# Kernel optimization log

Hardware: AMD Instinct MI355X
Metric: run time of the kernel (lower is better)

## Reference

```python
import jax, jax.numpy as jnp
import numpy as np

THR = 0.5
IOU_THR = 0.2
K = 4096          # fixed pre-NMS candidate budget (jit-compatible stand-in for thr filtering + full sort)
FEAT_OFF = 5      # cols: 0 obj score, 1:5 box (l,t,r,b), 5: class-feature embedding


def setup_inputs() -> dict:
    key = jax.random.key(0)
    kx, kl, kt, kw, kh, ks, kp, kr = jax.random.split(key, 8)
    C, H, W = 261, 320, 320  # 5 + 256 feature channels
    x = jax.random.normal(kx, (1, C, H, W), dtype=jnp.float32)
    # plausible (l,t,r,b) boxes in padded-image coordinates so NMS has real work
    l = jax.random.uniform(kl, (1, 1, H, W), dtype=jnp.float32) * 600.0
    t = jax.random.uniform(kt, (1, 1, H, W), dtype=jnp.float32) * 600.0
    r = l + jax.random.uniform(kw, (1, 1, H, W), dtype=jnp.float32) * 60.0
    b = t + jax.random.uniform(kh, (1, 1, H, W), dtype=jnp.float32) * 60.0
    x = x.at[:, 1:5].set(jnp.concatenate([l, t, r, b], axis=1))
    state_matrix = jax.random.normal(ks, (16, 256), dtype=jnp.float32)
    padding = jax.random.uniform(kp, (2,), dtype=jnp.float32) * 10.0
    ratio = jax.random.uniform(kr, (1,), dtype=jnp.float32) * 0.6 + 0.4
    return {"x": x, "state_matrix": state_matrix, "padding": padding,
            "ratio": ratio, "image_width": 1280, "image_height": 768}


def _pairwise_iou(boxes, eps=1e-10):
    # boxes: [K, 4] as (l, t, r, b); returns [K, K]
    l, t, r, b = boxes[:, 0], boxes[:, 1], boxes[:, 2], boxes[:, 3]
    area = (r - l) * (b - t)
    iw = jnp.clip(jnp.minimum(r[:, None], r[None, :]) - jnp.maximum(l[:, None], l[None, :]), 0.0)
    ih = jnp.clip(jnp.minimum(b[:, None], b[None, :]) - jnp.maximum(t[:, None], t[None, :]), 0.0)
    inter = iw * ih
    union = area[:, None] + area[None, :] - inter + eps
    return inter / union


def reference(x, state_matrix, padding, ratio, image_width, image_height):
    B, C, H, W = x.shape
    out = x[0].reshape(C, H * W).T                      # [N, C]
    sig = jax.nn.sigmoid(out[:, 0])                     # sigmoid on objectness channel
    cls_logits = out[:, FEAT_OFF:] @ state_matrix.T     # [N, 16] class-state matmul
    cls_val = jnp.max(cls_logits, axis=1)
    cls_idx = jnp.argmax(cls_logits, axis=1)
    score = sig * cls_val                               # out[:,0] * cls_values
    valid = sig > THR                                   # out[0] > thr filter
    score = jnp.where(valid, score, -jnp.inf)
    topv, topi = jax.lax.top_k(score, K)                # descending sort, fixed budget
    boxes = out[topi, 1:5]                              # [K, 4] (l,t,r,b)
    cls_k = cls_idx[topi]
    area = (boxes[:, 2] - boxes[:, 0]) * (boxes[:, 3] - boxes[:, 1])
    iou = _pairwise_iou(boxes)                          # [K, K]

    alive0 = jnp.isfinite(topv)                         # only thr-passing candidates enter the queue
    kept0 = jnp.zeros((K,), dtype=bool)

    def body(carry, i):
        alive, kept = carry
        is_cur = alive[i]                               # still in the queue (not suppressed earlier)
        alive = alive.at[i].set(False)                  # pop top
        ious_i = iou[i]
        n_over = jnp.sum((ious_i >= IOU_THR) & alive)   # remaining boxes with iou >= thr
        accept = is_cur & (area[i] >= 4.0) & (n_over >= 10)
        kept = kept.at[i].set(accept)
        alive = jnp.where(accept, alive & (ious_i < IOU_THR), alive)  # suppress only on accept
        return (alive, kept), None

    (_, kept), _ = jax.lax.scan(body, (alive0, kept0), jnp.arange(K))

    keep = kept & (topv >= THR)                         # p[0,0] < thr -> skip
    inv_r = 1.0 / ratio[0]
    x1 = jnp.maximum((boxes[:, 0] - padding[0]) * inv_r, 0.0)
    y1 = jnp.maximum((boxes[:, 1] - padding[1]) * inv_r, 0.0)
    x2 = jnp.minimum((boxes[:, 2] - padding[0]) * inv_r, jnp.float32(image_width))
    y2 = jnp.minimum((boxes[:, 3] - padding[1]) * inv_r, jnp.float32(image_height))
    keep = keep & (x1 < image_width) & (y1 < image_height)

    dets = jnp.stack([jnp.ones((K,), jnp.float32), topv, x1, y1, x2, y2,
                      cls_k.astype(jnp.float32)], axis=1)   # [K, 7]
    dets = jnp.where(keep[:, None], dets, 0.0)
    return dets
```

## Files before the change

### kernel.cpp

```cpp
#include <hip/hip_runtime.h>
#include <hip/hip_bf16.h>
#include <math.h>

#define HW 102400
#define KSEL 4096
#define CAP 16384

__device__ inline unsigned fkey(float f) {
    unsigned u = __float_as_uint(f);
    return (u & 0x80000000u) ? ~u : (u | 0x80000000u);
}

__device__ inline unsigned wave_sum64_s(unsigned x) {
    x += (unsigned)__builtin_amdgcn_update_dpp(0, (int)x, 0x111, 0xf, 0xf, false);
    x += (unsigned)__builtin_amdgcn_update_dpp(0, (int)x, 0x112, 0xf, 0xf, false);
    x += (unsigned)__builtin_amdgcn_update_dpp(0, (int)x, 0x114, 0xf, 0xf, false);
    x += (unsigned)__builtin_amdgcn_update_dpp(0, (int)x, 0x118, 0xf, 0xf, false);
    x += (unsigned)__builtin_amdgcn_update_dpp(0, (int)x, 0x142, 0xa, 0xf, false);
    x += (unsigned)__builtin_amdgcn_update_dpp(0, (int)x, 0x143, 0xc, 0xf, false);
    return (unsigned)__builtin_amdgcn_readlane((int)x, 63);
}

__device__ inline unsigned long long readlane64(unsigned long long v, int l) {
    unsigned lo = (unsigned)__builtin_amdgcn_readlane((int)(unsigned)(v & 0xffffffffull), l);
    unsigned hi = (unsigned)__builtin_amdgcn_readlane((int)(unsigned)(v >> 32), l);
    return ((unsigned long long)hi << 32) | lo;
}

__global__ __launch_bounds__(128) void k_score(const float* __restrict__ x,
                                               const float* __restrict__ sm,
                                               float* __restrict__ score,
                                               int* __restrict__ clsidx,
                                               unsigned* __restrict__ hist) {
    __shared__ float swt[256][16];
    __shared__ float tile[2][16][128];
    int t = threadIdx.x;
    for (int i = t; i < 4096; i += 128) {
        int k = i >> 8, c = i & 255;
        swt[c][k] = sm[i];
    }
    int cg = t >> 5;
    int le = t & 31;
    size_t pxb = (size_t)blockIdx.x * 128;
    const float* xc = x + (size_t)5 * HW + pxb;

    float acc[16];
#pragma unroll
    for (int k = 0; k < 16; ++k) acc[k] = 0.f;

    float4 sa[4], sb[4];

#define LOADX(dst, ti)                                                         \
    _Pragma("unroll") for (int j = 0; j < 4; ++j)                              \
        dst[j] = *(const float4*)(xc + (size_t)((ti) * 16 + 4 * j + cg) * HW + le * 4);
#define STOREX(src, s)                                                         \
    _Pragma("unroll") for (int j = 0; j < 4; ++j)                              \
        ((float4*)&tile[s][4 * j + cg][0])[le] = src[j];
#define COMP(s, ti)                                                            \
    _Pragma("unroll") for (int cc = 0; cc < 16; ++cc) {                        \
        float xv = tile[s][cc][t];                                             \
        const float4* w4 = (const float4*)&swt[(ti) * 16 + cc][0];             \
        float4 w0 = w4[0], w1 = w4[1], w2 = w4[2], w3 = w4[3];                 \
        acc[0]  = fmaf(xv, w0.x, acc[0]);  acc[1]  = fmaf(xv, w0.y, acc[1]);   \
        acc[2]  = fmaf(xv, w0.z, acc[2]);  acc[3]  = fmaf(xv, w0.w, acc[3]);   \
        acc[4]  = fmaf(xv, w1.x, acc[4]);  acc[5]  = fmaf(xv, w1.y, acc[5]);   \
        acc[6]  = fmaf(xv, w1.z, acc[6]);  acc[7]  = fmaf(xv, w1.w, acc[7]);   \
        acc[8]  = fmaf(xv, w2.x, acc[8]);  acc[9]  = fmaf(xv, w2.y, acc[9]);   \
        acc[10] = fmaf(xv, w2.z, acc[10]); acc[11] = fmaf(xv, w2.w, acc[11]);  \
        acc[12] = fmaf(xv, w3.x, acc[12]); acc[13] = fmaf(xv, w3.y, acc[13]);  \
        acc[14] = fmaf(xv, w3.z, acc[14]); acc[15] = fmaf(xv, w3.w, acc[15]);  \
    }

    LOADX(sa, 0);
    STOREX(sa, 0);
    LOADX(sa, 1);
    LOADX(sb, 2);
    __syncthreads();

#pragma unroll
    for (int k = 0; k < 16; k += 2) {
        COMP(k & 1, k);
        STOREX(sa, (k + 1) & 1);
        if (k + 3 < 16) LOADX(sa, k + 3);
        __syncthreads();
        COMP((k + 1) & 1, k + 1);
        if (k + 2 < 16) { STOREX(sb, k & 1); }
        if (k + 4 < 16) LOADX(sb, k + 4);
        __syncthreads();
    }
#undef LOADX
#undef STOREX
#undef COMP

    float mv = acc[0]; int mi = 0;
#pragma unroll
    for (int k = 1; k < 16; ++k)
        if (acc[k] > mv) { mv = acc[k]; mi = k; }
    int n = (int)pxb + t;
    float x0 = x[n];
    float sig = 1.0f / (1.0f + expf(-x0));
    float sc = (sig > 0.5f) ? sig * mv : -INFINITY;
    score[n] = sc;
    clsidx[n] = mi;
    if (sc != -INFINITY) atomicAdd(&hist[fkey(sc) >> 16], 1u);
}

__global__ __launch_bounds__(1024) void k_findp(const unsigned* __restrict__ hist,
                                                unsigned* __restrict__ meta) {
    __shared__ unsigned part[1024];
    __shared__ unsigned sgrp, s_after;
    __shared__ unsigned bins[64];
    int t = threadIdx.x;
    if (t == 0) { sgrp = 0; s_after = 0; }
    unsigned s = 0;
    const unsigned* hp = hist + t * 64;
    for (int i = 0; i < 64; ++i) s += hp[i];
    part[t] = s;
    __syncthreads();
    for (int off = 1; off < 1024; off <<= 1) {
        unsigned v = (t + off < 1024) ? part[t + off] : 0u;
        __syncthreads();
        part[t] += v;
        __syncthreads();
    }
    if (part[t] >= KSEL && (t == 1023 || part[t + 1] < KSEL)) {
        sgrp = (unsigned)t;
        s_after = (t == 1023) ? 0u : part[t + 1];
    }
    __syncthreads();
    unsigned g = sgrp, SA = s_after;
    if (t < 64) bins[t] = hist[g * 64 + t];
    __syncthreads();
    if (t == 0) {
        unsigned acc = SA, p = g * 64;
        for (int b = 63; b >= 0; --b) {
            acc += bins[b];
            if (acc >= KSEL) { p = g * 64 + (unsigned)b; break; }
        }
        meta[1] = p;
    }
}

__global__ void k_collect(const float* __restrict__ score,
                          unsigned* __restrict__ meta,
                          unsigned long long* __restrict__ cand) {
    int n = blockIdx.x * 256 + threadIdx.x;
    unsigned key = fkey(score[n]);
    if ((key >> 16) >= meta[1]) {
        unsigned pos = atomicAdd(&meta[0], 1u);
        if (pos < CAP)
            cand[pos] = ((unsigned long long)key << 32) | (unsigned)(~(unsigned)n);
    }
}

__global__ __launch_bounds__(256) void k_rank(const unsigned long long* __restrict__ cand,
                                              const unsigned* __restrict__ meta,
                                              const float* __restrict__ x,
                                              const float* __restrict__ score,
                                              const int* __restrict__ clsidx,
                                              float* __restrict__ topv,
                                              float* __restrict__ bl, float* __restrict__ bt,
                                              float* __restrict__ br, float* __restrict__ bb,
                                              float* __restrict__ area, int* __restrict__ clsk) {
    __shared__ unsigned long long tile[1024];
    int C = (int)meta[0]; if (C > CAP) C = CAP;
    int j = blockIdx.x * 256 + threadIdx.x;
    unsigned long long kj = (j < C) ? cand[j] : 0ull;
    unsigned rank = 0;
    for (int tb = 0; tb < C; tb += 1024) {
        int cnt = min(1024, C - tb);
        __syncthreads();
        for (int u = threadIdx.x; u < cnt; u += 256) tile[u] = cand[tb + u];
        __syncthreads();
        if (j < C)
            for (int u = 0; u < cnt; ++u) rank += (tile[u] > kj) ? 1u : 0u;
    }
    if (j < C && rank < KSEL) {
        unsigned n = ~(unsigned)(kj & 0xFFFFFFFFull);
        float l  = x[(size_t)1 * HW + n];
        float tt = x[(size_t)2 * HW + n];
        float r  = x[(size_t)3 * HW + n];
        float b  = x[(size_t)4 * HW + n];
        topv[rank] = score[n];
        bl[rank] = l; bt[rank] = tt; br[rank] = r; bb[rank] = b;
        area[rank] = (r - l) * (b - tt);
        clsk[rank] = clsidx[n];
    }
}

__global__ __launch_bounds__(256) void k_mask(const float* __restrict__ bl, const float* __restrict__ bt,
                                              const float* __restrict__ br, const float* __restrict__ bb,
                                              const float* __restrict__ area,
                                              unsigned long long* __restrict__ mask) {
    __shared__ float sl[256], st[256], sr[256], sb[256], sa[256];
    int t = threadIdx.x;
    int ic = blockIdx.x >> 4;
    int jc = blockIdx.x & 15;
    int i = ic * 256 + t;
    int j0 = jc * 256;
    sl[t] = bl[j0 + t]; st[t] = bt[j0 + t]; sr[t] = br[j0 + t];
    sb[t] = bb[j0 + t]; sa[t] = area[j0 + t];
    __syncthreads();
    float li = bl[i], ti = bt[i], ri = br[i], bi = bb[i], ai = area[i];
#pragma unroll
    for (int w = 0; w < 4; ++w) {
        unsigned long long m = 0;
        for (int k2 = 0; k2 < 64; ++k2) {
            int j = w * 64 + k2;
            float iw = fminf(ri, sr[j]) - fmaxf(li, sl[j]); iw = fmaxf(iw, 0.f);
            float ih = fminf(bi, sb[j]) - fmaxf(ti, st[j]); ih = fmaxf(ih, 0.f);
            float inter = iw * ih;
            float uni = ai + sa[j] - inter + 1e-10f;
            if (inter / uni >= 0.2f) m |= (1ull << k2);
        }
        mask[(size_t)i * 64 + (jc * 4 + w)] = m;
    }
}

__global__ __launch_bounds__(256, 1) void k_nms(const unsigned long long* __restrict__ mask,
                                                const float* __restrict__ topv,
                                                const float* __restrict__ area,
                                                const float* __restrict__ bl, const float* __restrict__ bt,
                                                const float* __restrict__ br, const float* __restrict__ bb,
                                                const int* __restrict__ clsk,
                                                const float* __restrict__ padding,
                                                const float* __restrict__ ratio,
                                                const int* __restrict__ piw, const int* __restrict__ pih,
                                                float* __restrict__ out) {
    __shared__ unsigned long long rowsL[2][4096];
    __shared__ unsigned long long aliveL[64];
    __shared__ unsigned long long keptL[64];
    __shared__ unsigned cntL[64];
    int t = threadIdx.x;
    int lane = t & 63;
    int W = t >> 6;
    int g = t & 3;
    int jrow = t >> 2;

    unsigned long long alive = 0, areaok = 0, keptAcc = 0;
    if (W == 0) {
        for (int k = 0; k < 64; ++k) {
            float tv = topv[(size_t)k * 64 + lane];
            float ar = area[(size_t)k * 64 + lane];
            unsigned long long b1 = __ballot(tv != -INFINITY);
            unsigned long long b2 = __ballot(ar >= 4.0f);
            if (lane == k) { alive = b1; areaok = b2; }
        }
        aliveL[lane] = alive;
    }

#define STAGE(bb, s)                                                            \
    do {                                                                        \
        _Pragma("unroll") for (int i = 0; i < 8; ++i) {                         \
            int seg_ = i * 4 + W;                                               \
            int r_ = seg_ * 2 + (lane >> 5);                                    \
            int p_ = (lane & 31) * 2;                                           \
            int wl_ = (p_ - 2 * r_) & 63;                                       \
            const unsigned long long* gp_ =                                     \
                mask + ((size_t)((bb) * 64 + r_) * 64 + wl_);                   \
            __builtin_amdgcn_global_load_lds(                                   \
                (const __attribute__((address_space(1))) void*)gp_,             \
                (__attribute__((address_space(3))) void*)&rowsL[s][seg_ * 128], \
                16, 0, 0);                                                      \
        }                                                                       \
    } while (0)

    STAGE(0, 0);
    STAGE(1, 1);

#define VER(jj, rw)                                                             \
    {                                                                           \
        unsigned long long awc = readlane64(alive, b);                          \
        if ((awc >> (jj)) & 1ull) {                                             \
            unsigned long long awAdj = alive;                                   \
            unsigned long long pm = ((jj) == 63) ? ~0ull                        \
                                                 : ((1ull << ((jj) + 1)) - 1ull); \
            if (lane == b) awAdj &= ~pm;                                        \
            unsigned c_ = (unsigned)__popcll((rw) & awAdj);                     \
            unsigned tt_ = wave_sum64_s(c_);                                    \
            if (tt_ >= 10u) { alive &= ~(rw); keptB |= 1ull << (jj); }          \
        }                                                                       \
    }

    for (int b = 0; b < 64; ++b) {
        if (b < 63) asm volatile("s_waitcnt vmcnt(8)" ::: "memory");
        else        asm volatile("s_waitcnt vmcnt(0)" ::: "memory");
        __builtin_amdgcn_sched_barrier(0);
        __builtin_amdgcn_s_barrier();

        const unsigned long long* rb = &rowsL[b & 1][0];

        unsigned long long pfxj = (jrow == 63) ? ~0ull : ((1ull << (jrow + 1)) - 1ull);
        int base_w = g * 16;
        unsigned cnt = 0;
#pragma unroll
        for (int q = 0; q < 8; ++q) {
            int wl = base_w + q * 2;
            int ph = (wl + 2 * jrow) & 63;
            ulonglong2 rv = *(const ulonglong2*)&rb[jrow * 64 + ph];
            ulonglong2 av = *(const ulonglong2*)&aliveL[wl];
            unsigned cx = (unsigned)__popcll(rv.x & av.x);
            unsigned cy = (unsigned)__popcll(rv.y & av.y);
            cnt += cx + cy;
            if (wl == b)     cnt -= (unsigned)__popcll(rv.x & av.x & pfxj);
            if (wl + 1 == b) cnt -= (unsigned)__popcll(rv.y & av.y & pfxj);
        }
        cnt += (unsigned)__builtin_amdgcn_update_dpp(0, (int)cnt, 0xB1, 0xf, 0xf, false);
        cnt += (unsigned)__builtin_amdgcn_update_dpp(0, (int)cnt, 0x4E, 0xf, 0xf, false);
        if (g == 0) cntL[jrow] = cnt;
        asm volatile("s_waitcnt lgkmcnt(0)" ::: "memory");
        __builtin_amdgcn_s_barrier();

        if (W == 0) {
            unsigned long long keptB = 0;
            unsigned long long aw0snap = readlane64(alive, b);
            unsigned long long areaok0 = readlane64(areaok, b);
            unsigned myc = cntL[lane];
            bool candp = (myc >= 10u) && ((areaok0 >> lane) & 1ull) &&
                         ((aw0snap >> lane) & 1ull);
            unsigned long long cand = __ballot(candp);
            while (cand) {
                int j1 = __ffsll(cand) - 1; cand &= cand - 1;
                int j2 = -1, j3 = -1, j4 = -1;
                if (cand) { j2 = __ffsll(cand) - 1; cand &= cand - 1; }
                if (cand) { j3 = __ffsll(cand) - 1; cand &= cand - 1; }
                if (cand) { j4 = __ffsll(cand) - 1; cand &= cand - 1; }
                unsigned long long r1 = rb[j1 * 64 + ((lane + 2 * j1) & 63)];
                unsigned long long r2 = (j2 >= 0) ? rb[j2 * 64 + ((lane + 2 * j2) & 63)] : 0;
                unsigned long long r3 = (j3 >= 0) ? rb[j3 * 64 + ((lane + 2 * j3) & 63)] : 0;
                unsigned long long r4 = (j4 >= 0) ? rb[j4 * 64 + ((lane + 2 * j4) & 63)] : 0;
                VER(j1, r1);
                if (j2 >= 0) VER(j2, r2);
                if (j3 >= 0) VER(j3, r3);
                if (j4 >= 0) VER(j4, r4);
            }
            if (lane == b) { alive = 0; keptAcc = keptB; }
            aliveL[lane] = alive;
        }
        asm volatile("s_waitcnt lgkmcnt(0)" ::: "memory");
        __builtin_amdgcn_s_barrier();
        if (b + 2 < 64) STAGE(b + 2, b & 1);
    }
    if (W == 0) keptL[lane] = keptAcc;
    __syncthreads();

    float p0 = padding[0], p1 = padding[1];
    float invr = 1.0f / ratio[0];
    float Wimg = (float)piw[0], Himg = (float)pih[0];
    for (int i = t; i < KSEL; i += 256) {
        bool kept = (keptL[i >> 6] >> (i & 63)) & 1ull;
        float tv = topv[i];
        bool keep = kept && (tv >= 0.5f);
        float x1 = fmaxf((bl[i] - p0) * invr, 0.f);
        float y1 = fmaxf((bt[i] - p1) * invr, 0.f);
        float x2 = fminf((br[i] - p0) * invr, Wimg);
        float y2 = fminf((bb[i] - p1) * invr, Himg);
        keep = keep && (x1 < Wimg) && (y1 < Himg);
        float* o = out + (size_t)i * 7;
        if (keep) {
            o[0] = 1.0f; o[1] = tv; o[2] = x1; o[3] = y1; o[4] = x2; o[5] = y2;
            o[6] = (float)clsk[i];
        } else {
            o[0] = 0.f; o[1] = 0.f; o[2] = 0.f; o[3] = 0.f; o[4] = 0.f; o[5] = 0.f; o[6] = 0.f;
        }
    }
#undef STAGE
#undef VER
}

extern "C" void kernel_launch(void* const* d_in, const int* in_sizes, int n_in,
                              void* d_out, int out_size, void* d_ws, size_t ws_size,
                              hipStream_t stream) {
    const float* x       = (const float*)d_in[0];
    const float* sm      = (const float*)d_in[1];
    const float* padding = (const float*)d_in[2];
    const float* ratio   = (const float*)d_in[3];
    const int*   piw     = (const int*)d_in[4];
    const int*   pih     = (const int*)d_in[5];
    float* out = (float*)d_out;
    char* ws = (char*)d_ws;

    float* score               = (float*)(ws + 0);
    int*   clsidx              = (int*)(ws + 409600);
    unsigned* hist             = (unsigned*)(ws + 819200);
    unsigned* meta             = (unsigned*)(ws + 1081344);
    unsigned long long* cand   = (unsigned long long*)(ws + 1081856);
    float* topv                = (float*)(ws + 1212928);
    float* bl                  = (float*)(ws + 1229312);
    float* bt                  = (float*)(ws + 1245696);
    float* br                  = (float*)(ws + 1262080);
    float* bb                  = (float*)(ws + 1278464);
    float* area                = (float*)(ws + 1294848);
    int*   clsk                = (int*)(ws + 1311232);
    unsigned long long* mask   = (unsigned long long*)(ws + 1328128);

    hipMemsetAsync(hist, 0, 262144 + 512, stream);

    k_score  <<<800, 128, 0, stream>>>(x, sm, score, clsidx, hist);
    k_findp  <<<1, 1024, 0, stream>>>(hist, meta);
    k_collect<<<400, 256, 0, stream>>>(score, meta, cand);
    k_rank   <<<CAP / 256, 256, 0, stream>>>(cand, meta, x, score, clsidx,
                                             topv, bl, bt, br, bb, area, clsk);
    k_mask   <<<256, 256, 0, stream>>>(bl, bt, br, bb, area, mask);
    k_nms    <<<1, 256, 0, stream>>>(mask, topv, area, bl, bt, br, bb, clsk,
                                     padding, ratio, piw, pih, out);
}
```

Before: 312.2 us.

## Specialize NMS waves: wave0 prefetches and resolves, waves 1-3 count overlaps

Restructures the serial NMS block loop with warp specialization. Wave 0 alone issues the async global-to-LDS mask row loads into a triple buffer and runs the sequential verification. Waves 1-3 split the 64 mask words into three column ranges, skip rows that are no longer alive, and write partial counts that wave 0 sums. The alive/areaok ballot setup is also spread across all four waves. The intent is to overlap mask prefetch with the count phase and cut redundant counting work, at the cost of more LDS and the count work running on three waves instead of four.

```diff
diff --git a/kernel.cpp b/kernel.cpp
--- a/kernel.cpp
+++ b/kernel.cpp
@@ -227,46 +227,29 @@
                                                 const float* __restrict__ ratio,
                                                 const int* __restrict__ piw, const int* __restrict__ pih,
                                                 float* __restrict__ out) {
-    __shared__ unsigned long long rowsL[2][4096];
+    __shared__ unsigned long long rowsL[3][4096];
     __shared__ unsigned long long aliveL[64];
+    __shared__ unsigned long long areaokL[64];
     __shared__ unsigned long long keptL[64];
-    __shared__ unsigned cntL[64];
+    __shared__ unsigned cntL[64][3];
     int t = threadIdx.x;
     int lane = t & 63;
     int W = t >> 6;
-    int g = t & 3;
-    int jrow = t >> 2;
-
-    unsigned long long alive = 0, areaok = 0, keptAcc = 0;
-    if (W == 0) {
-        for (int k = 0; k < 64; ++k) {
-            float tv = topv[(size_t)k * 64 + lane];
-            float ar = area[(size_t)k * 64 + lane];
-            unsigned long long b1 = __ballot(tv != -INFINITY);
-            unsigned long long b2 = __ballot(ar >= 4.0f);
-            if (lane == k) { alive = b1; areaok = b2; }
-        }
-        aliveL[lane] = alive;
-    }
-
-#define STAGE(bb, s)                                                            \
+
+#define STAGE0(bb, s)                                                           \
     do {                                                                        \
-        _Pragma("unroll") for (int i = 0; i < 8; ++i) {                         \
-            int seg_ = i * 4 + W;                                               \
-            int r_ = seg_ * 2 + (lane >> 5);                                    \
+        _Pragma("unroll") for (int i_ = 0; i_ < 32; ++i_) {                     \
+            int r_ = i_ * 2 + (lane >> 5);                                      \
             int p_ = (lane & 31) * 2;                                           \
             int wl_ = (p_ - 2 * r_) & 63;                                       \
             const unsigned long long* gp_ =                                     \
                 mask + ((size_t)((bb) * 64 + r_) * 64 + wl_);                   \
             __builtin_amdgcn_global_load_lds(                                   \
                 (const __attribute__((address_space(1))) void*)gp_,             \
-                (__attribute__((address_space(3))) void*)&rowsL[s][seg_ * 128], \
+                (__attribute__((address_space(3))) void*)&rowsL[s][i_ * 128],   \
                 16, 0, 0);                                                      \
         }                                                                       \
     } while (0)
-
-    STAGE(0, 0);
-    STAGE(1, 1);
 
 #define VER(jj, rw)                                                             \
     {                                                                           \
@@ -282,40 +265,65 @@
         }                                                                       \
     }
 
+#pragma unroll
+    for (int kk = 0; kk < 16; ++kk) {
+        int k = W * 16 + kk;
+        float tv = topv[(size_t)k * 64 + lane];
+        float ar = area[(size_t)k * 64 + lane];
+        unsigned long long b1 = __ballot(tv != -INFINITY);
+        unsigned long long b2 = __ballot(ar >= 4.0f);
+        if (lane == 0) { aliveL[k] = b1; areaokL[k] = b2; }
+    }
+    asm volatile("s_waitcnt lgkmcnt(0)" ::: "memory");
+    __builtin_amdgcn_sched_barrier(0);
+    __builtin_amdgcn_s_barrier();
+
+    unsigned long long alive = 0, areaok = 0, keptAcc = 0;
+    if (W == 0) {
+        alive  = aliveL[lane];
+        areaok = areaokL[lane];
+        STAGE0(0, 0);
+        STAGE0(1, 1);
+        asm volatile("s_waitcnt vmcnt(32)" ::: "memory");
+    }
+    __builtin_amdgcn_sched_barrier(0);
+    __builtin_amdgcn_s_barrier();
+
     for (int b = 0; b < 64; ++b) {
-        if (b < 63) asm volatile("s_waitcnt vmcnt(8)" ::: "memory");
-        else        asm volatile("s_waitcnt vmcnt(0)" ::: "memory");
+        if (W == 0) {
+            if (b + 2 < 64) STAGE0(b + 2, (b + 2) % 3);
+        } else {
+            const unsigned long long* rb = &rowsL[b % 3][0];
+            int j = lane;
+            unsigned long long aliveB = aliveL[b];
+            if ((aliveB >> j) & 1ull) {
+                unsigned long long pfxj = (j == 63) ? ~0ull : ((1ull << (j + 1)) - 1ull);
+                int base = (W == 1) ? 0 : (W == 2) ? 22 : 44;
+                int np   = (W == 3) ? 10 : 11;
+                unsigned cnt = 0;
+                for (int q = 0; q < np; ++q) {
+                    int wl = base + 2 * q;
+                    int ph = (wl + 2 * j) & 63;
+                    ulonglong2 rv = *(const ulonglong2*)&rb[j * 64 + ph];
+                    ulonglong2 av = *(const ulonglong2*)&aliveL[wl];
+                    unsigned long long ax = rv.x & av.x, ay = rv.y & av.y;
+                    cnt += (unsigned)__popcll(ax) + (unsigned)__popcll(ay);
+                    if (wl == b)     cnt -= (unsigned)__popcll(ax & pfxj);
+                    if (wl + 1 == b) cnt -= (unsigned)__popcll(ay & pfxj);
+                }
+                cntL[j][W - 1] = cnt;
+            }
+        }
+        asm volatile("s_waitcnt lgkmcnt(0)" ::: "memory");
         __builtin_amdgcn_sched_barrier(0);
         __builtin_amdgcn_s_barrier();
 
-        const unsigned long long* rb = &rowsL[b & 1][0];
-
-        unsigned long long pfxj = (jrow == 63) ? ~0ull : ((1ull << (jrow + 1)) - 1ull);
-        int base_w = g * 16;
-        unsigned cnt = 0;
-#pragma unroll
-        for (int q = 0; q < 8; ++q) {
-            int wl = base_w + q * 2;
-            int ph = (wl + 2 * jrow) & 63;
-            ulonglong2 rv = *(const ulonglong2*)&rb[jrow * 64 + ph];
-            ulonglong2 av = *(const ulonglong2*)&aliveL[wl];
-            unsigned cx = (unsigned)__popcll(rv.x & av.x);
-            unsigned cy = (unsigned)__popcll(rv.y & av.y);
-            cnt += cx + cy;
-            if (wl == b)     cnt -= (unsigned)__popcll(rv.x & av.x & pfxj);
-            if (wl + 1 == b) cnt -= (unsigned)__popcll(rv.y & av.y & pfxj);
-        }
-        cnt += (unsigned)__builtin_amdgcn_update_dpp(0, (int)cnt, 0xB1, 0xf, 0xf, false);
-        cnt += (unsigned)__builtin_amdgcn_update_dpp(0, (int)cnt, 0x4E, 0xf, 0xf, false);
-        if (g == 0) cntL[jrow] = cnt;
-        asm volatile("s_waitcnt lgkmcnt(0)" ::: "memory");
-        __builtin_amdgcn_s_barrier();
-
         if (W == 0) {
+            const unsigned long long* rb = &rowsL[b % 3][0];
             unsigned long long keptB = 0;
             unsigned long long aw0snap = readlane64(alive, b);
             unsigned long long areaok0 = readlane64(areaok, b);
-            unsigned myc = cntL[lane];
+            unsigned myc = cntL[lane][0] + cntL[lane][1] + cntL[lane][2];
             bool candp = (myc >= 10u) && ((areaok0 >> lane) & 1ull) &&
                          ((aw0snap >> lane) & 1ull);
             unsigned long long cand = __ballot(candp);
@@ -336,10 +344,12 @@
             }
             if (lane == b) { alive = 0; keptAcc = keptB; }
             aliveL[lane] = alive;
+            asm volatile("s_waitcnt lgkmcnt(0)" ::: "memory");
+            if (b < 62) asm volatile("s_waitcnt vmcnt(32)" ::: "memory");
+            else        asm volatile("s_waitcnt vmcnt(0)" ::: "memory");
         }
-        asm volatile("s_waitcnt lgkmcnt(0)" ::: "memory");
+        __builtin_amdgcn_sched_barrier(0);
         __builtin_amdgcn_s_barrier();
-        if (b + 2 < 64) STAGE(b + 2, b & 1);
     }
     if (W == 0) keptL[lane] = keptAcc;
     __syncthreads();
@@ -364,7 +374,7 @@
             o[0] = 0.f; o[1] = 0.f; o[2] = 0.f; o[3] = 0.f; o[4] = 0.f; o[5] = 0.f; o[6] = 0.f;
         }
     }
-#undef STAGE
+#undef STAGE0
 #undef VER
 }
 
```

Result: no change. 313.0 us, median of 2 (+0.2%).

## Fuse all pipeline stages into one persistent kernel with grid barriers

Applied to the files above, without the earlier changes.

Replaces the six separate kernel launches (score, threshold find, collect, rank, IoU mask, NMS) with a single 400-block kernel that moves between stages through atomic-counter grid barriers. The threshold search is made redundant per block: each block reads the histogram and computes the pivot itself instead of running a separate single-block kernel. The goal is to remove launch gaps and inter-kernel drain. The cost is spin-wait barriers that need all 400 blocks co-resident, a large shared-memory footprint per block, and idle blocks in the later stages.

```diff
diff --git a/kernel.cpp b/kernel.cpp
--- a/kernel.cpp
+++ b/kernel.cpp
@@ -5,6 +5,7 @@
 #define HW 102400
 #define KSEL 4096
 #define CAP 16384
+#define NB 400
 
 __device__ inline unsigned fkey(float f) {
     unsigned u = __float_as_uint(f);
@@ -27,35 +28,55 @@
     return ((unsigned long long)hi << 32) | lo;
 }
 
-__global__ __launch_bounds__(128) void k_score(const float* __restrict__ x,
-                                               const float* __restrict__ sm,
-                                               float* __restrict__ score,
-                                               int* __restrict__ clsidx,
-                                               unsigned* __restrict__ hist) {
-    __shared__ float swt[256][16];
-    __shared__ float tile[2][16][128];
-    int t = threadIdx.x;
-    for (int i = t; i < 4096; i += 128) {
-        int k = i >> 8, c = i & 255;
-        swt[c][k] = sm[i];
-    }
-    int cg = t >> 5;
-    int le = t & 31;
-    size_t pxb = (size_t)blockIdx.x * 128;
-    const float* xc = x + (size_t)5 * HW + pxb;
-
-    float acc[16];
+__device__ inline void gridbar(unsigned* slot, unsigned nb) {
+    __syncthreads();
+    __threadfence();
+    if (threadIdx.x == 0) {
+        atomicAdd(slot, 1u);
+        while (atomicAdd(slot, 0u) < nb) { __builtin_amdgcn_s_sleep(8); }
+    }
+    __syncthreads();
+    __threadfence();
+}
+
+__global__ __launch_bounds__(256, 2) void k_all(
+        const float* __restrict__ x, const float* __restrict__ sm,
+        float* __restrict__ score, int* __restrict__ clsidx,
+        unsigned* __restrict__ hist, unsigned* __restrict__ meta,
+        unsigned long long* __restrict__ cand,
+        float* __restrict__ topv, float* __restrict__ bl, float* __restrict__ bt,
+        float* __restrict__ br, float* __restrict__ bb, float* __restrict__ area,
+        int* __restrict__ clsk, unsigned long long* __restrict__ mask,
+        const float* __restrict__ padding, const float* __restrict__ ratio,
+        const int* __restrict__ piw, const int* __restrict__ pih,
+        float* __restrict__ out) {
+    __shared__ __align__(16) char smem[69632];
+    const int t = threadIdx.x;
+    const int b = blockIdx.x;
+    unsigned* bar = meta + 8;
+
+    {
+        float (*swt)[16] = (float(*)[16])smem;
+        float (*tile)[16][256] = (float(*)[16][256])(smem + 16384);
+        for (int i = t; i < 4096; i += 256) {
+            int k = i >> 8, c = i & 255;
+            swt[c][k] = sm[i];
+        }
+        int wave = t >> 6, lane = t & 63;
+        size_t pxb = (size_t)b * 256;
+        const float* xc = x + (size_t)5 * HW + pxb;
+
+        float acc[16];
 #pragma unroll
-    for (int k = 0; k < 16; ++k) acc[k] = 0.f;
-
-    float4 sa[4], sb[4];
+        for (int k = 0; k < 16; ++k) acc[k] = 0.f;
+        float4 sa[4], sb[4];
 
 #define LOADX(dst, ti)                                                         \
     _Pragma("unroll") for (int j = 0; j < 4; ++j)                              \
-        dst[j] = *(const float4*)(xc + (size_t)((ti) * 16 + 4 * j + cg) * HW + le * 4);
+        dst[j] = *(const float4*)(xc + (size_t)((ti) * 16 + wave * 4 + j) * HW + lane * 4);
 #define STOREX(src, s)                                                         \
     _Pragma("unroll") for (int j = 0; j < 4; ++j)                              \
-        ((float4*)&tile[s][4 * j + cg][0])[le] = src[j];
+        ((float4*)&tile[s][wave * 4 + j][0])[lane] = src[j];
 #define COMP(s, ti)                                                            \
     _Pragma("unroll") for (int cc = 0; cc < 16; ++cc) {                        \
         float xv = tile[s][cc][t];                                             \
@@ -70,302 +91,285 @@
         acc[12] = fmaf(xv, w3.x, acc[12]); acc[13] = fmaf(xv, w3.y, acc[13]);  \
         acc[14] = fmaf(xv, w3.z, acc[14]); acc[15] = fmaf(xv, w3.w, acc[15]);  \
     }
-
-    LOADX(sa, 0);
-    STOREX(sa, 0);
-    LOADX(sa, 1);
-    LOADX(sb, 2);
-    __syncthreads();
-
+        LOADX(sa, 0);
+        STOREX(sa, 0);
+        LOADX(sa, 1);
+        LOADX(sb, 2);
+        __syncthreads();
 #pragma unroll
-    for (int k = 0; k < 16; k += 2) {
-        COMP(k & 1, k);
-        STOREX(sa, (k + 1) & 1);
-        if (k + 3 < 16) LOADX(sa, k + 3);
-        __syncthreads();
-        COMP((k + 1) & 1, k + 1);
-        if (k + 2 < 16) { STOREX(sb, k & 1); }
-        if (k + 4 < 16) LOADX(sb, k + 4);
-        __syncthreads();
-    }
+        for (int k = 0; k < 16; k += 2) {
+            COMP(k & 1, k);
+            STOREX(sa, (k + 1) & 1);
+            if (k + 3 < 16) LOADX(sa, k + 3);
+            __syncthreads();
+            COMP((k + 1) & 1, k + 1);
+            if (k + 2 < 16) { STOREX(sb, k & 1); }
+            if (k + 4 < 16) LOADX(sb, k + 4);
+            __syncthreads();
+        }
 #undef LOADX
 #undef STOREX
 #undef COMP
-
-    float mv = acc[0]; int mi = 0;
+        float mv = acc[0]; int mi = 0;
 #pragma unroll
-    for (int k = 1; k < 16; ++k)
-        if (acc[k] > mv) { mv = acc[k]; mi = k; }
-    int n = (int)pxb + t;
-    float x0 = x[n];
-    float sig = 1.0f / (1.0f + expf(-x0));
-    float sc = (sig > 0.5f) ? sig * mv : -INFINITY;
-    score[n] = sc;
-    clsidx[n] = mi;
-    if (sc != -INFINITY) atomicAdd(&hist[fkey(sc) >> 16], 1u);
-}
-
-__global__ __launch_bounds__(1024) void k_findp(const unsigned* __restrict__ hist,
-                                                unsigned* __restrict__ meta) {
-    __shared__ unsigned part[1024];
-    __shared__ unsigned sgrp, s_after;
-    __shared__ unsigned bins[64];
-    int t = threadIdx.x;
-    if (t == 0) { sgrp = 0; s_after = 0; }
-    unsigned s = 0;
-    const unsigned* hp = hist + t * 64;
-    for (int i = 0; i < 64; ++i) s += hp[i];
-    part[t] = s;
-    __syncthreads();
-    for (int off = 1; off < 1024; off <<= 1) {
-        unsigned v = (t + off < 1024) ? part[t + off] : 0u;
-        __syncthreads();
-        part[t] += v;
-        __syncthreads();
-    }
-    if (part[t] >= KSEL && (t == 1023 || part[t + 1] < KSEL)) {
-        sgrp = (unsigned)t;
-        s_after = (t == 1023) ? 0u : part[t + 1];
-    }
-    __syncthreads();
-    unsigned g = sgrp, SA = s_after;
-    if (t < 64) bins[t] = hist[g * 64 + t];
-    __syncthreads();
-    if (t == 0) {
-        unsigned acc = SA, p = g * 64;
-        for (int b = 63; b >= 0; --b) {
-            acc += bins[b];
-            if (acc >= KSEL) { p = g * 64 + (unsigned)b; break; }
-        }
-        meta[1] = p;
-    }
-}
-
-__global__ void k_collect(const float* __restrict__ score,
-                          unsigned* __restrict__ meta,
-                          unsigned long long* __restrict__ cand) {
-    int n = blockIdx.x * 256 + threadIdx.x;
-    unsigned key = fkey(score[n]);
-    if ((key >> 16) >= meta[1]) {
-        unsigned pos = atomicAdd(&meta[0], 1u);
-        if (pos < CAP)
-            cand[pos] = ((unsigned long long)key << 32) | (unsigned)(~(unsigned)n);
-    }
-}
-
-__global__ __launch_bounds__(256) void k_rank(const unsigned long long* __restrict__ cand,
-                                              const unsigned* __restrict__ meta,
-                                              const float* __restrict__ x,
-                                              const float* __restrict__ score,
-                                              const int* __restrict__ clsidx,
-                                              float* __restrict__ topv,
-                                              float* __restrict__ bl, float* __restrict__ bt,
-                                              float* __restrict__ br, float* __restrict__ bb,
-                                              float* __restrict__ area, int* __restrict__ clsk) {
-    __shared__ unsigned long long tile[1024];
-    int C = (int)meta[0]; if (C > CAP) C = CAP;
-    int j = blockIdx.x * 256 + threadIdx.x;
-    unsigned long long kj = (j < C) ? cand[j] : 0ull;
-    unsigned rank = 0;
-    for (int tb = 0; tb < C; tb += 1024) {
-        int cnt = min(1024, C - tb);
-        __syncthreads();
-        for (int u = threadIdx.x; u < cnt; u += 256) tile[u] = cand[tb + u];
-        __syncthreads();
-        if (j < C)
-            for (int u = 0; u < cnt; ++u) rank += (tile[u] > kj) ? 1u : 0u;
-    }
-    if (j < C && rank < KSEL) {
-        unsigned n = ~(unsigned)(kj & 0xFFFFFFFFull);
-        float l  = x[(size_t)1 * HW + n];
-        float tt = x[(size_t)2 * HW + n];
-        float r  = x[(size_t)3 * HW + n];
-        float b  = x[(size_t)4 * HW + n];
-        topv[rank] = score[n];
-        bl[rank] = l; bt[rank] = tt; br[rank] = r; bb[rank] = b;
-        area[rank] = (r - l) * (b - tt);
-        clsk[rank] = clsidx[n];
-    }
-}
-
-__global__ __launch_bounds__(256) void k_mask(const float* __restrict__ bl, const float* __restrict__ bt,
-                                              const float* __restrict__ br, const float* __restrict__ bb,
-                                              const float* __restrict__ area,
-                                              unsigned long long* __restrict__ mask) {
-    __shared__ float sl[256], st[256], sr[256], sb[256], sa[256];
-    int t = threadIdx.x;
-    int ic = blockIdx.x >> 4;
-    int jc = blockIdx.x & 15;
-    int i = ic * 256 + t;
-    int j0 = jc * 256;
-    sl[t] = bl[j0 + t]; st[t] = bt[j0 + t]; sr[t] = br[j0 + t];
-    sb[t] = bb[j0 + t]; sa[t] = area[j0 + t];
-    __syncthreads();
-    float li = bl[i], ti = bt[i], ri = br[i], bi = bb[i], ai = area[i];
+        for (int k = 1; k < 16; ++k)
+            if (acc[k] > mv) { mv = acc[k]; mi = k; }
+        int n = (int)pxb + t;
+        float x0 = x[n];
+        float sig = 1.0f / (1.0f + expf(-x0));
+        float sc = (sig > 0.5f) ? sig * mv : -INFINITY;
+        score[n] = sc;
+        clsidx[n] = mi;
+        if (sc != -INFINITY) atomicAdd(&hist[fkey(sc) >> 16], 1u);
+    }
+    gridbar(&bar[0], NB);
+
+    unsigned p16;
+    {
+        unsigned* part = (unsigned*)smem;
+        unsigned* shr  = (unsigned*)(smem + 1024);
+        if (t == 0) { shr[0] = 0; shr[1] = 0; }
+        unsigned s = 0;
+        const uint4* hp4 = (const uint4*)(hist + (size_t)t * 256);
+#pragma unroll 8
+        for (int i = 0; i < 64; ++i) { uint4 v = hp4[i]; s += v.x + v.y + v.z + v.w; }
+        part[t] = s;
+        __syncthreads();
+        for (int off = 1; off < 256; off <<= 1) {
+            unsigned v = (t + off < 256) ? part[t + off] : 0u;
+            __syncthreads();
+            part[t] += v;
+            __syncthreads();
+        }
+        if (part[t] >= KSEL && (t == 255 || part[t + 1] < KSEL)) {
+            shr[0] = (unsigned)t;
+            shr[1] = (t == 255) ? 0u : part[t + 1];
+        }
+        __syncthreads();
+        if (t == 0) {
+            unsigned g = shr[0], acc = shr[1], p = g * 256;
+            for (int b2 = 255; b2 >= 0; --b2) {
+                acc += hist[g * 256 + b2];
+                if (acc >= KSEL) { p = g * 256 + (unsigned)b2; break; }
+            }
+            shr[2] = p;
+        }
+        __syncthreads();
+        p16 = shr[2];
+        __syncthreads();
+    }
+
+    {
+        int n = b * 256 + t;
+        unsigned key = fkey(score[n]);
+        if ((key >> 16) >= p16) {
+            unsigned pos = atomicAdd(&meta[0], 1u);
+            if (pos < CAP)
+                cand[pos] = ((unsigned long long)key << 32) | (unsigned)(~(unsigned)n);
+        }
+    }
+    gridbar(&bar[1], NB);
+
+    if (b < 64) {
+        unsigned long long* tile64 = (unsigned long long*)smem;
+        int C = (int)meta[0]; if (C > CAP) C = CAP;
+        int j = b * 256 + t;
+        unsigned long long kj = (j < C) ? cand[j] : 0ull;
+        unsigned rank = 0;
+        for (int tb = 0; tb < C; tb += 1024) {
+            int cnt = min(1024, C - tb);
+            __syncthreads();
+            for (int u = t; u < cnt; u += 256) tile64[u] = cand[tb + u];
+            __syncthreads();
+            if (j < C)
+                for (int u = 0; u < cnt; ++u) rank += (tile64[u] > kj) ? 1u : 0u;
+        }
+        if (j < C && rank < KSEL) {
+            unsigned n = ~(unsigned)(kj & 0xFFFFFFFFull);
+            float l  = x[(size_t)1 * HW + n];
+            float tt = x[(size_t)2 * HW + n];
+            float r  = x[(size_t)3 * HW + n];
+            float bo = x[(size_t)4 * HW + n];
+            topv[rank] = score[n];
+            bl[rank] = l; bt[rank] = tt; br[rank] = r; bb[rank] = bo;
+            area[rank] = (r - l) * (bo - tt);
+            clsk[rank] = clsidx[n];
+        }
+    }
+    gridbar(&bar[2], NB);
+
+    if (b < 256) {
+        float* sl = (float*)smem;
+        float* stt = (float*)(smem + 1024);
+        float* sr = (float*)(smem + 2048);
+        float* sbb = (float*)(smem + 3072);
+        float* saa = (float*)(smem + 4096);
+        int ic = b >> 4;
+        int jc = b & 15;
+        int i = ic * 256 + t;
+        int j0 = jc * 256;
+        sl[t] = bl[j0 + t]; stt[t] = bt[j0 + t]; sr[t] = br[j0 + t];
+        sbb[t] = bb[j0 + t]; saa[t] = area[j0 + t];
+        __syncthreads();
+        float li = bl[i], ti = bt[i], ri = br[i], bi = bb[i], ai = area[i];
 #pragma unroll
-    for (int w = 0; w < 4; ++w) {
-        unsigned long long m = 0;
-        for (int k2 = 0; k2 < 64; ++k2) {
-            int j = w * 64 + k2;
-            float iw = fminf(ri, sr[j]) - fmaxf(li, sl[j]); iw = fmaxf(iw, 0.f);
-            float ih = fminf(bi, sb[j]) - fmaxf(ti, st[j]); ih = fmaxf(ih, 0.f);
-            float inter = iw * ih;
-            float uni = ai + sa[j] - inter + 1e-10f;
-            if (inter / uni >= 0.2f) m |= (1ull << k2);
-        }
-        mask[(size_t)i * 64 + (jc * 4 + w)] = m;
-    }
-}
-
-__global__ __launch_bounds__(256, 1) void k_nms(const unsigned long long* __restrict__ mask,
-                                                const float* __restrict__ topv,
-                                                const float* __restrict__ area,
-                                                const float* __restrict__ bl, const float* __restrict__ bt,
-                                                const float* __restrict__ br, const float* __restrict__ bb,
-                                                const int* __restrict__ clsk,
-                                                const float* __restrict__ padding,
-                                                const float* __restrict__ ratio,
-                                                const int* __restrict__ piw, const int* __restrict__ pih,
-                                                float* __restrict__ out) {
-    __shared__ unsigned long long rowsL[2][4096];
-    __shared__ unsigned long long aliveL[64];
-    __shared__ unsigned long long keptL[64];
-    __shared__ unsigned cntL[64];
-    int t = threadIdx.x;
-    int lane = t & 63;
-    int W = t >> 6;
-    int g = t & 3;
-    int jrow = t >> 2;
-
-    unsigned long long alive = 0, areaok = 0, keptAcc = 0;
-    if (W == 0) {
-        for (int k = 0; k < 64; ++k) {
-            float tv = topv[(size_t)k * 64 + lane];
-            float ar = area[(size_t)k * 64 + lane];
-            unsigned long long b1 = __ballot(tv != -INFINITY);
-            unsigned long long b2 = __ballot(ar >= 4.0f);
-            if (lane == k) { alive = b1; areaok = b2; }
-        }
-        aliveL[lane] = alive;
-    }
-
-#define STAGE(bb, s)                                                            \
+        for (int w = 0; w < 4; ++w) {
+            unsigned long long m = 0;
+            for (int k2 = 0; k2 < 64; ++k2) {
+                int j = w * 64 + k2;
+                float iw = fminf(ri, sr[j]) - fmaxf(li, sl[j]); iw = fmaxf(iw, 0.f);
+                float ih = fminf(bi, sbb[j]) - fmaxf(ti, stt[j]); ih = fmaxf(ih, 0.f);
+                float inter = iw * ih;
+                float uni = ai + saa[j] - inter + 1e-10f;
+                if (inter / uni >= 0.2f) m |= (1ull << k2);
+            }
+            mask[(size_t)i * 64 + (jc * 4 + w)] = m;
+        }
+        __syncthreads();
+    }
+    gridbar(&bar[3], NB);
+    if (b != 0) return;
+
+    {
+        unsigned long long* rowsF = (unsigned long long*)smem;
+        unsigned long long* aliveL = (unsigned long long*)(smem + 65536);
+        unsigned long long* keptL  = (unsigned long long*)(smem + 66048);
+        unsigned* cntF = (unsigned*)(smem + 66560);
+        int lane = t & 63;
+        int W = t >> 6;
+        int g = t & 3;
+        int jrow = t >> 2;
+
+#define STAGEF(bb2, s)                                                          \
     do {                                                                        \
-        _Pragma("unroll") for (int i = 0; i < 8; ++i) {                         \
-            int seg_ = i * 4 + W;                                               \
+        _Pragma("unroll") for (int i_ = 0; i_ < 8; ++i_) {                      \
+            int seg_ = i_ * 4 + W;                                              \
             int r_ = seg_ * 2 + (lane >> 5);                                    \
             int p_ = (lane & 31) * 2;                                           \
             int wl_ = (p_ - 2 * r_) & 63;                                       \
             const unsigned long long* gp_ =                                     \
-                mask + ((size_t)((bb) * 64 + r_) * 64 + wl_);                   \
+                mask + ((size_t)((bb2) * 64 + r_) * 64 + wl_);                  \
             __builtin_amdgcn_global_load_lds(                                   \
                 (const __attribute__((address_space(1))) void*)gp_,             \
-                (__attribute__((address_space(3))) void*)&rowsL[s][seg_ * 128], \
+                (__attribute__((address_space(3))) void*)&rowsF[(s) * 4096 + seg_ * 128], \
                 16, 0, 0);                                                      \
         }                                                                       \
     } while (0)
 
-    STAGE(0, 0);
-    STAGE(1, 1);
-
-#define VER(jj, rw)                                                             \
+#define VERF(jj, rw)                                                            \
     {                                                                           \
-        unsigned long long awc = readlane64(alive, b);                          \
+        unsigned long long awc = readlane64(alive, bq);                         \
         if ((awc >> (jj)) & 1ull) {                                             \
             unsigned long long awAdj = alive;                                   \
             unsigned long long pm = ((jj) == 63) ? ~0ull                        \
                                                  : ((1ull << ((jj) + 1)) - 1ull); \
-            if (lane == b) awAdj &= ~pm;                                        \
+            if (lane == bq) awAdj &= ~pm;                                       \
             unsigned c_ = (unsigned)__popcll((rw) & awAdj);                     \
             unsigned tt_ = wave_sum64_s(c_);                                    \
             if (tt_ >= 10u) { alive &= ~(rw); keptB |= 1ull << (jj); }          \
         }                                                                       \
     }
 
-    for (int b = 0; b < 64; ++b) {
-        if (b < 63) asm volatile("s_waitcnt vmcnt(8)" ::: "memory");
-        else        asm volatile("s_waitcnt vmcnt(0)" ::: "memory");
-        __builtin_amdgcn_sched_barrier(0);
-        __builtin_amdgcn_s_barrier();
-
-        const unsigned long long* rb = &rowsL[b & 1][0];
-
-        unsigned long long pfxj = (jrow == 63) ? ~0ull : ((1ull << (jrow + 1)) - 1ull);
-        int base_w = g * 16;
-        unsigned cnt = 0;
+        STAGEF(0, 0);
+        STAGEF(1, 1);
+
+        unsigned long long alive = 0, areaok = 0, keptAcc = 0;
+        if (W == 0) {
+            for (int k = 0; k < 64; ++k) {
+                float tv = topv[(size_t)k * 64 + lane];
+                float ar = area[(size_t)k * 64 + lane];
+                unsigned long long b1 = __ballot(tv != -INFINITY);
+                unsigned long long b2 = __ballot(ar >= 4.0f);
+                if (lane == k) { alive = b1; areaok = b2; }
+            }
+            aliveL[lane] = alive;
+        }
+
+        for (int bq = 0; bq < 64; ++bq) {
+            if (bq < 63) asm volatile("s_waitcnt vmcnt(8)" ::: "memory");
+            else         asm volatile("s_waitcnt vmcnt(0)" ::: "memory");
+            __builtin_amdgcn_sched_barrier(0);
+            __builtin_amdgcn_s_barrier();
+
+            const unsigned long long* rb = &rowsF[(bq & 1) * 4096];
+
+            unsigned long long pfxj = (jrow == 63) ? ~0ull : ((1ull << (jrow + 1)) - 1ull);
+            int base_w = g * 16;
+            unsigned cnt = 0;
 #pragma unroll
-        for (int q = 0; q < 8; ++q) {
-            int wl = base_w + q * 2;
-            int ph = (wl + 2 * jrow) & 63;
-            ulonglong2 rv = *(const ulonglong2*)&rb[jrow * 64 + ph];
-            ulonglong2 av = *(const ulonglong2*)&aliveL[wl];
-            unsigned cx = (unsigned)__popcll(rv.x & av.x);
-            unsigned cy = (unsigned)__popcll(rv.y & av.y);
-            cnt += cx + cy;
-            if (wl == b)     cnt -= (unsigned)__popcll(rv.x & av.x & pfxj);
-            if (wl + 1 == b) cnt -= (unsigned)__popcll(rv.y & av.y & pfxj);
-        }
-        cnt += (unsigned)__builtin_amdgcn_update_dpp(0, (int)cnt, 0xB1, 0xf, 0xf, false);
-        cnt += (unsigned)__builtin_amdgcn_update_dpp(0, (int)cnt, 0x4E, 0xf, 0xf, false);
-        if (g == 0) cntL[jrow] = cnt;
-        asm volatile("s_waitcnt lgkmcnt(0)" ::: "memory");
-        __builtin_amdgcn_s_barrier();
-
-        if (W == 0) {
-            unsigned long long keptB = 0;
-            unsigned long long aw0snap = readlane64(alive, b);
-            unsigned long long areaok0 = readlane64(areaok, b);
-            unsigned myc = cntL[lane];
-            bool candp = (myc >= 10u) && ((areaok0 >> lane) & 1ull) &&
-                         ((aw0snap >> lane) & 1ull);
-            unsigned long long cand = __ballot(candp);
-            while (cand) {
-                int j1 = __ffsll(cand) - 1; cand &= cand - 1;
-                int j2 = -1, j3 = -1, j4 = -1;
-                if (cand) { j2 = __ffsll(cand) - 1; cand &= cand - 1; }
-                if (cand) { j3 = __ffsll(cand) - 1; cand &= cand - 1; }
-                if (cand) { j4 = __ffsll(cand) - 1; cand &= cand - 1; }
-                unsigned long long r1 = rb[j1 * 64 + ((lane + 2 * j1) & 63)];
-                unsigned long long r2 = (j2 >= 0) ? rb[j2 * 64 + ((lane + 2 * j2) & 63)] : 0;
-                unsigned long long r3 = (j3 >= 0) ? rb[j3 * 64 + ((lane + 2 * j3) & 63)] : 0;
-                unsigned long long r4 = (j4 >= 0) ? rb[j4 * 64 + ((lane + 2 * j4) & 63)] : 0;
-                VER(j1, r1);
-                if (j2 >= 0) VER(j2, r2);
-                if (j3 >= 0) VER(j3, r3);
-                if (j4 >= 0) VER(j4, r4);
-            }
-            if (lane == b) { alive = 0; keptAcc = keptB; }
-            aliveL[lane] = alive;
-        }
-        asm volatile("s_waitcnt lgkmcnt(0)" ::: "memory");
-        __builtin_amdgcn_s_barrier();
-        if (b + 2 < 64) STAGE(b + 2, b & 1);
-    }
-    if (W == 0) keptL[lane] = keptAcc;
-    __syncthreads();
-
-    float p0 = padding[0], p1 = padding[1];
-    float invr = 1.0f / ratio[0];
-    float Wimg = (float)piw[0], Himg = (float)pih[0];
-    for (int i = t; i < KSEL; i += 256) {
-        bool kept = (keptL[i >> 6] >> (i & 63)) & 1ull;
-        float tv = topv[i];
-        bool keep = kept && (tv >= 0.5f);
-        float x1 = fmaxf((bl[i] - p0) * invr, 0.f);
-        float y1 = fmaxf((bt[i] - p1) * invr, 0.f);
-        float x2 = fminf((br[i] - p0) * invr, Wimg);
-        float y2 = fminf((bb[i] - p1) * invr, Himg);
-        keep = keep && (x1 < Wimg) && (y1 < Himg);
-        float* o = out + (size_t)i * 7;
-        if (keep) {
-            o[0] = 1.0f; o[1] = tv; o[2] = x1; o[3] = y1; o[4] = x2; o[5] = y2;
-            o[6] = (float)clsk[i];
-        } else {
-            o[0] = 0.f; o[1] = 0.f; o[2] = 0.f; o[3] = 0.f; o[4] = 0.f; o[5] = 0.f; o[6] = 0.f;
-        }
-    }
-#undef STAGE
-#undef VER
+            for (int q = 0; q < 8; ++q) {
+                int wl = base_w + q * 2;
+                int ph = (wl + 2 * jrow) & 63;
+                ulonglong2 rv = *(const ulonglong2*)&rb[jrow * 64 + ph];
+                ulonglong2 av = *(const ulonglong2*)&aliveL[wl];
+                unsigned cx = (unsigned)__popcll(rv.x & av.x);
+                unsigned cy = (unsigned)__popcll(rv.y & av.y);
+                cnt += cx + cy;
+                if (wl == bq)     cnt -= (unsigned)__popcll(rv.x & av.x & pfxj);
+                if (wl + 1 == bq) cnt -= (unsigned)__popcll(rv.y & av.y & pfxj);
+            }
+            cnt += (unsigned)__builtin_amdgcn_update_dpp(0, (int)cnt, 0xB1, 0xf, 0xf, false);
+            cnt += (unsigned)__builtin_amdgcn_update_dpp(0, (int)cnt, 0x4E, 0xf, 0xf, false);
+            if (g == 0) cntF[jrow] = cnt;
+            asm volatile("s_waitcnt lgkmcnt(0)" ::: "memory");
+            __builtin_amdgcn_s_barrier();
+
+            if (W == 0) {
+                unsigned long long keptB = 0;
+                unsigned long long aw0snap = readlane64(alive, bq);
+                unsigned long long areaok0 = readlane64(areaok, bq);
+                unsigned myc = cntF[lane];
+                bool candp = (myc >= 10u) && ((areaok0 >> lane) & 1ull) &&
+                             ((aw0snap >> lane) & 1ull);
+                unsigned long long cq = __ballot(candp);
+                while (cq) {
+                    int j1 = __ffsll(cq) - 1; cq &= cq - 1;
+                    int j2 = -1, j3 = -1, j4 = -1;
+                    if (cq) { j2 = __ffsll(cq) - 1; cq &= cq - 1; }
+                    if (cq) { j3 = __ffsll(cq) - 1; cq &= cq - 1; }
+                    if (cq) { j4 = __ffsll(cq) - 1; cq &= cq - 1; }
+                    unsigned long long r1 = rb[j1 * 64 + ((lane + 2 * j1) & 63)];
+                    unsigned long long r2 = (j2 >= 0) ? rb[j2 * 64 + ((lane + 2 * j2) & 63)] : 0;
+                    unsigned long long r3 = (j3 >= 0) ? rb[j3 * 64 + ((lane + 2 * j3) & 63)] : 0;
+                    unsigned long long r4 = (j4 >= 0) ? rb[j4 * 64 + ((lane + 2 * j4) & 63)] : 0;
+                    VERF(j1, r1);
+                    if (j2 >= 0) VERF(j2, r2);
+                    if (j3 >= 0) VERF(j3, r3);
+                    if (j4 >= 0) VERF(j4, r4);
+                }
+                if (lane == bq) { alive = 0; keptAcc = keptB; }
+                aliveL[lane] = alive;
+            }
+            asm volatile("s_waitcnt lgkmcnt(0)" ::: "memory");
+            __builtin_amdgcn_s_barrier();
+            if (bq + 2 < 64) STAGEF(bq + 2, bq & 1);
+        }
+        if (W == 0) keptL[lane] = keptAcc;
+        __syncthreads();
+
+        float p0 = padding[0], p1 = padding[1];
+        float invr = 1.0f / ratio[0];
+        float Wimg = (float)piw[0], Himg = (float)pih[0];
+        for (int i = t; i < KSEL; i += 256) {
+            bool kept = (keptL[i >> 6] >> (i & 63)) & 1ull;
+            float tv = topv[i];
+            bool keep = kept && (tv >= 0.5f);
+            float x1 = fmaxf((bl[i] - p0) * invr, 0.f);
+            float y1 = fmaxf((bt[i] - p1) * invr, 0.f);
+            float x2 = fminf((br[i] - p0) * invr, Wimg);
+            float y2 = fminf((bb[i] - p1) * invr, Himg);
+            keep = keep && (x1 < Wimg) && (y1 < Himg);
+            float* o = out + (size_t)i * 7;
+            if (keep) {
+                o[0] = 1.0f; o[1] = tv; o[2] = x1; o[3] = y1; o[4] = x2; o[5] = y2;
+                o[6] = (float)clsk[i];
+            } else {
+                o[0] = 0.f; o[1] = 0.f; o[2] = 0.f; o[3] = 0.f; o[4] = 0.f; o[5] = 0.f; o[6] = 0.f;
+            }
+        }
+#undef STAGEF
+#undef VERF
+    }
 }
 
 extern "C" void kernel_launch(void* const* d_in, const int* in_sizes, int n_in,
@@ -396,12 +400,7 @@
 
     hipMemsetAsync(hist, 0, 262144 + 512, stream);
 
-    k_score  <<<800, 128, 0, stream>>>(x, sm, score, clsidx, hist);
-    k_findp  <<<1, 1024, 0, stream>>>(hist, meta);
-    k_collect<<<400, 256, 0, stream>>>(score, meta, cand);
-    k_rank   <<<CAP / 256, 256, 0, stream>>>(cand, meta, x, score, clsidx,
-                                             topv, bl, bt, br, bb, area, clsk);
-    k_mask   <<<256, 256, 0, stream>>>(bl, bt, br, bb, area, mask);
-    k_nms    <<<1, 256, 0, stream>>>(mask, topv, area, bl, bt, br, bb, clsk,
-                                     padding, ratio, piw, pih, out);
-}
+    k_all<<<NB, 256, 0, stream>>>(x, sm, score, clsidx, hist, meta, cand,
+                                  topv, bl, bt, br, bb, area, clsk, mask,
+                                  padding, ratio, piw, pih, out);
+}
```

After: 594.3 us. 1.9x slower.
